# Kernel optimization log

Hardware: AMD Instinct MI355X
Metric: run time of the kernel (lower is better)

Reference implementation:

```python
import jax, jax.numpy as jnp
import numpy as np

HEADS = 8
IH, IW = 32, 32
C_IN, C_OUT = 512, 512


def setup_inputs() -> dict:
    key = jax.random.key(0)
    k1, k2, k3, k4, k5 = jax.random.split(key, 5)
    B = 32
    n = IH + IW + (IH // 2) * (IW // 2)  # pooled kv length = 320
    x = jax.random.normal(k1, (B, C_IN, IH, IW), dtype=jnp.float32)
    # 1x1 conv weights stored as [out, in] (bias-free qkv, biased output proj)
    Wqkv = jax.random.normal(k2, (3 * C_IN, C_IN), dtype=jnp.float32) * 0.02
    Wout = jax.random.normal(k3, (C_OUT, C_IN), dtype=jnp.float32) * 0.02
    bout = jnp.zeros((C_OUT,), dtype=jnp.float32)
    pos_embed = jax.random.normal(k4, (1, IH * IW, n), dtype=jnp.float32) * 0.2
    return {"x": x, "Wqkv": Wqkv, "Wout": Wout, "bout": bout, "pos_embed": pos_embed}


def _pool_gate(t, B, C, H, W):
    # adaptive_avg_pool2d(.,(None,1)) == mean over width -> [B,C,H]
    th = t.mean(axis=3)
    # adaptive_avg_pool2d(.,(1,None)) (+permute) == mean over height -> [B,C,W]
    tw = t.mean(axis=2)
    # adaptive_avg_pool2d to (H//2, W//2) with even dims == 2x2 average pooling
    tp = t.reshape(B, C, H // 2, 2, W // 2, 2).mean(axis=(3, 5)).reshape(B, C, -1)
    s = jax.nn.sigmoid(jnp.concatenate([th, tw, tp], axis=2))  # [B,C,n]
    d = C // HEADS
    # 'b (h d) n -> b h n d'
    return s.reshape(B, HEADS, d, -1).transpose(0, 1, 3, 2)


def reference(x, Wqkv, Wout, bout, pos_embed):
    B, C, H, W = x.shape
    d = C // HEADS
    scale = d ** (-0.5)
    qkv = jnp.einsum('bchw,oc->bohw', x, Wqkv)  # 1x1 conv, no bias
    q, k, v = jnp.split(qkv, 3, axis=1)
    # 'b (h d) ih iw -> b h (ih iw) d'
    q = q.reshape(B, HEADS, d, H * W).transpose(0, 1, 3, 2)
    k = _pool_gate(k, B, C, H, W)  # [B,h,n,d]
    v = _pool_gate(v, B, C, H, W)  # [B,h,n,d]
    dots = jnp.einsum('bhsd,bhnd->bhsn', q, k) * scale + pos_embed  # pos_embed [1,s,n] broadcasts
    attn = jax.nn.softmax(dots, axis=-1)
    out = jnp.einsum('bhsn,bhnd->bhsd', attn, v)
    # 'b h (ih iw) d -> b (h d) ih iw'
    out = out.transpose(0, 1, 3, 2).reshape(B, HEADS * d, H, W)
    out = jnp.einsum('bchw,oc->bohw', out, Wout) + bout[None, :, None, None]
    return out
```

## Files before the change

kernel.cpp:

```cpp
#include <hip/hip_runtime.h>
#include <hip/hip_bf16.h>
#include <math.h>

#define HEADS 8
#define CH    512
#define S     1024
#define NKV   320
#define DH    64
#define BATCH 32

typedef __attribute__((ext_vector_type(8))) short short8;
typedef __attribute__((ext_vector_type(4))) short short4v;
typedef __attribute__((ext_vector_type(4))) float float4v;
typedef __attribute__((ext_vector_type(4))) unsigned int uint4v;

__device__ __forceinline__ short f2bf(float f) {
    __hip_bfloat16 h = __float2bfloat16(f);
    return *reinterpret_cast<short*>(&h);
}

#define GLOAD_LDS16(gp, lp) __builtin_amdgcn_global_load_lds( \
    (const __attribute__((address_space(1))) void*)(gp),      \
    (__attribute__((address_space(3))) void*)(lp), 16, 0, 0)

__global__ __launch_bounds__(256) void pool_kernel(const float* __restrict__ x,
                                                   float* __restrict__ xp) {
    __shared__ float sm[4][1024];
    const int w = threadIdx.x >> 6;
    const int l = threadIdx.x & 63;
    const int p = blockIdx.x * 4 + w;
    const float* src = x + (size_t)p * 1024;
    #pragma unroll
    for (int j = 0; j < 16; ++j) sm[w][j * 64 + l] = src[j * 64 + l];
    __syncthreads();
    float* dst = xp + (size_t)p * NKV;
    const float* pl = sm[w];
    #pragma unroll
    for (int g = 0; g < 5; ++g) {
        const int nn = g * 64 + l;
        float r;
        if (nn < 32) {
            const int h = nn; float s = 0.f;
            #pragma unroll
            for (int ww = 0; ww < 32; ++ww) s += pl[h * 32 + ww];
            r = s * (1.0f / 32.0f);
        } else if (nn < 64) {
            const int ww = nn - 32; float s = 0.f;
            #pragma unroll
            for (int h = 0; h < 32; ++h) s += pl[h * 32 + ww];
            r = s * (1.0f / 32.0f);
        } else {
            const int i = nn - 64;
            const int ph = i >> 4, pw = i & 15;
            r = 0.25f * (pl[(2 * ph) * 32 + 2 * pw]     + pl[(2 * ph) * 32 + 2 * pw + 1] +
                         pl[(2 * ph + 1) * 32 + 2 * pw] + pl[(2 * ph + 1) * 32 + 2 * pw + 1]);
        }
        dst[nn] = r;
    }
}

__global__ __launch_bounds__(256) void tcast(const float* __restrict__ in,
                                             short* __restrict__ out, int R, int C) {
    __shared__ float sm[64][65];
    const int t = threadIdx.x;
    const int c0 = blockIdx.x * 64, r0 = blockIdx.y * 64;
    const float* ib = in + ((size_t)blockIdx.z * R + r0) * C + c0;
    #pragma unroll
    for (int rep = 0; rep < 4; ++rep) {
        const int r = rep * 16 + (t >> 4), c = (t & 15) * 4;
        const float4 v = *(const float4*)&ib[(size_t)r * C + c];
        sm[r][c] = v.x; sm[r][c + 1] = v.y; sm[r][c + 2] = v.z; sm[r][c + 3] = v.w;
    }
    __syncthreads();
    short* ob = out + ((size_t)blockIdx.z * C + c0) * R + r0;
    #pragma unroll
    for (int rep = 0; rep < 4; ++rep) {
        const int cr = rep * 16 + (t >> 4), rc = (t & 15) * 4;
        short4v p;
        #pragma unroll
        for (int e = 0; e < 4; ++e) p[e] = f2bf(sm[rc + e][cr]);
        *(short4v*)&ob[(size_t)cr * R + rc] = p;
    }
}

__global__ __launch_bounds__(256) void castw(const float* __restrict__ in,
                                             short* __restrict__ out, int n) {
    const int i = (blockIdx.x * 256 + threadIdx.x) * 4;
    if (i < n) {
        const float4 v = *(const float4*)&in[i];
        short4v p = {f2bf(v.x), f2bf(v.y), f2bf(v.z), f2bf(v.w)};
        *(short4v*)&out[i] = p;
    }
}

template <int MT, int NT, int ACT, typename OT>
__global__ __launch_bounds__(256) void gemm_bf16(const short* __restrict__ A, long sAb,
                                                 const short* __restrict__ B, long sBb,
                                                 const float* __restrict__ bias,
                                                 OT* __restrict__ C, int M, int N) {
    constexpr int K  = 512;
    constexpr int BM = 32 * MT, BN = 32 * NT;
    __shared__ short As[BM * 64];
    __shared__ short Bs[BN * 64];
    const int t = threadIdx.x, w = t >> 6, l = t & 63;
    const int wm = w >> 1, wn = w & 1, quad = l >> 4, m15 = l & 15;
    const int bz = blockIdx.z;
    const int n0 = blockIdx.x * BN, m0 = blockIdx.y * BM;
    const short* gA = A + (size_t)sAb * bz + (size_t)m0 * K;
    const short* gB = B + (size_t)sBb * bz + (size_t)n0 * K;
    const int lrow = l >> 3;
    const int pc   = l & 7;

    const float4v zf = {0.f, 0.f, 0.f, 0.f};
    float4v acc[MT][NT];
    #pragma unroll
    for (int i = 0; i < MT; ++i)
        #pragma unroll
        for (int j = 0; j < NT; ++j) acc[i][j] = zf;

    for (int k0 = 0; k0 < K; k0 += 64) {
        #pragma unroll
        for (int ii = w; ii < BM / 8; ii += 4) {
            const int row = ii * 8 + lrow;
            const int x = pc ^ (row & 7);
            GLOAD_LDS16(gA + (size_t)row * K + k0 + x * 8, &As[ii * 512]);
        }
        #pragma unroll
        for (int ii = w; ii < BN / 8; ii += 4) {
            const int row = ii * 8 + lrow;
            const int x = pc ^ (row & 7);
            GLOAD_LDS16(gB + (size_t)row * K + k0 + x * 8, &Bs[ii * 512]);
        }
        __syncthreads();
        #pragma unroll
        for (int ks = 0; ks < 2; ++ks) {
            const int xa = (((ks * 4 + quad) ^ (m15 & 7))) * 8;
            short8 aF[MT], bF[NT];
            #pragma unroll
            for (int i = 0; i < MT; ++i)
                aF[i] = *(const short8*)&As[((wm * MT + i) * 16 + m15) * 64 + xa];
            #pragma unroll
            for (int j = 0; j < NT; ++j)
                bF[j] = *(const short8*)&Bs[((wn * NT + j) * 16 + m15) * 64 + xa];
            #pragma unroll
            for (int i = 0; i < MT; ++i)
                #pragma unroll
                for (int j = 0; j < NT; ++j)
                    acc[i][j] = __builtin_amdgcn_mfma_f32_16x16x32_bf16(aF[i], bF[j], acc[i][j], 0, 0, 0);
        }
        __syncthreads();
    }

    OT* gC = C + (size_t)bz * M * N;
    #pragma unroll
    for (int i = 0; i < MT; ++i) {
        #pragma unroll
        for (int r = 0; r < 4; ++r) {
            const int row = m0 + (wm * MT + i) * 16 + quad * 4 + r;
            float bv = 0.f;
            if (ACT == 2) bv = bias[row];
            #pragma unroll
            for (int j = 0; j < NT; ++j) {
                const int col = n0 + (wn * NT + j) * 16 + m15;
                float v = acc[i][j][r];
                if (ACT == 1) { v = 1.0f / (1.0f + __expf(-v)); if (col < 512) v *= 0.125f; }
                if (ACT == 2) v += bv;
                if constexpr (sizeof(OT) == 2)
                    ((short*)gC)[(size_t)row * N + col] = f2bf(v);
                else
                    ((float*)gC)[(size_t)row * N + col] = v;
            }
        }
    }
}

__global__ __launch_bounds__(512, 6) void attn_mfma(const short* __restrict__ qT,
                                                    const short* __restrict__ kvT,
                                                    const float* __restrict__ pos,
                                                    short* __restrict__ aoT) {
    __shared__ short smB[64 * 320];
    const int tid = threadIdx.x, w = tid >> 6, l = tid & 63;
    const int quad = l >> 4, m15 = l & 15;
    const int b = blockIdx.z, h = blockIdx.y, s0 = blockIdx.x * 128;
    const short* kvb = kvT + (size_t)b * NKV * 1024;

    const int nperm = (l & 35) | ((l & 12) << 1) | ((l & 16) >> 2);
    #pragma unroll
    for (int i2 = w; i2 < 40; i2 += 8) {
        const int nb = i2 % 5, dg = i2 / 5;
        GLOAD_LDS16(kvb + (size_t)(nb * 64 + nperm) * 1024 + h * 64 + dg * 8,
                    &smB[(dg * 320 + nb * 64) * 8]);
    }
    const short* qb = qT + (size_t)(b * S + s0 + w * 16 + m15) * 512 + h * 64;
    const short8 aQ0 = *(const short8*)&qb[quad * 8];
    const short8 aQ1 = *(const short8*)&qb[32 + quad * 8];
    __syncthreads();

    const float* posrow = pos + (size_t)(s0 + w * 16 + m15) * NKV + quad * 8;
    unsigned int P[40];
    float lpart = 0.f;
    #pragma unroll
    for (int tt = 0; tt < 20; ++tt) {
        float4v a = {0.f, 0.f, 0.f, 0.f};
        const short8 k0 = *(const short8*)&smB[(quad * 320 + tt * 16 + m15) * 8];
        const short8 k1 = *(const short8*)&smB[((4 + quad) * 320 + tt * 16 + m15) * 8];
        a = __builtin_amdgcn_mfma_f32_16x16x32_bf16(k0, aQ0, a, 0, 0, 0);
        a = __builtin_amdgcn_mfma_f32_16x16x32_bf16(k1, aQ1, a, 0, 0, 0);
        const int n0 = (tt >> 2) * 64 + ((tt >> 1) & 1) * 32 + (tt & 1) * 4;
        const float4 pv = *(const float4*)&posrow[n0];
        const float p0 = __expf(a[0] + pv.x);
        const float p1 = __expf(a[1] + pv.y);
        const float p2 = __expf(a[2] + pv.z);
        const float p3 = __expf(a[3] + pv.w);
        lpart += (p0 + p1) + (p2 + p3);
        P[tt * 2]     = (unsigned int)(unsigned short)f2bf(p0) |
                        ((unsigned int)(unsigned short)f2bf(p1) << 16);
        P[tt * 2 + 1] = (unsigned int)(unsigned short)f2bf(p2) |
                        ((unsigned int)(unsigned short)f2bf(p3) << 16);
    }

    float lrow = lpart;
    lrow += __shfl_xor(lrow, 16, 64);
    lrow += __shfl_xor(lrow, 32, 64);
    const float invl = 1.0f / lrow;
    float inv[4];
    #pragma unroll
    for (int r = 0; r < 4; ++r)
        inv[r] = __shfl(invl, (l & 48) | (quad * 4 + r), 64);

    __syncthreads();

    for (int it = 0; it < 5; ++it) {
        const int i2 = it * 512 + tid;
        const int n5 = i2 & 31, d8 = (i2 >> 5) & 7, nb = i2 >> 8;
        const int n = nb * 32 + n5;
        const short8 v = *(const short8*)&kvb[(size_t)n * 1024 + 512 + h * 64 + d8 * 8];
        const int x = n >> 3;
        #pragma unroll
        for (int e = 0; e < 8; ++e)
            smB[(d8 * 8 + e) * 320 + ((x ^ e) * 8) + (n & 7)] = v[e];
    }
    __syncthreads();

    const float4v zf = {0.f, 0.f, 0.f, 0.f};
    #pragma unroll
    for (int half = 0; half < 2; ++half) {
        float4v O0 = zf, O1 = zf;
        #pragma unroll
        for (int c = 0; c < 5; ++c) {
            const uint4v u0 = {P[c * 8 + 0], P[c * 8 + 1], P[c * 8 + 2], P[c * 8 + 3]};
            const uint4v u1 = {P[c * 8 + 4], P[c * 8 + 5], P[c * 8 + 6], P[c * 8 + 7]};
            const short8 aP0 = __builtin_bit_cast(short8, u0);
            const short8 aP1 = __builtin_bit_cast(short8, u1);
            #pragma unroll
            for (int ks = 0; ks < 2; ++ks) {
                const int xr = (c * 8 + ks * 4 + quad) ^ (m15 & 7);
                const int dt0 = half * 2;
                const short8 bV0 = *(const short8*)&smB[(dt0 * 16 + m15) * 320 + xr * 8];
                const short8 bV1 = *(const short8*)&smB[((dt0 + 1) * 16 + m15) * 320 + xr * 8];
                if (ks == 0) {
                    O0 = __builtin_amdgcn_mfma_f32_16x16x32_bf16(aP0, bV0, O0, 0, 0, 0);
                    O1 = __builtin_amdgcn_mfma_f32_16x16x32_bf16(aP0, bV1, O1, 0, 0, 0);
                } else {
                    O0 = __builtin_amdgcn_mfma_f32_16x16x32_bf16(aP1, bV0, O0, 0, 0, 0);
                    O1 = __builtin_amdgcn_mfma_f32_16x16x32_bf16(aP1, bV1, O1, 0, 0, 0);
                }
            }
        }
        #pragma unroll
        for (int r = 0; r < 4; ++r) {
            const int s = s0 + w * 16 + quad * 4 + r;
            short* orow = &aoT[(size_t)(b * S + s) * 512 + h * 64 + (half * 2) * 16 + m15];
            orow[0]  = f2bf(O0[r] * inv[r]);
            orow[16] = f2bf(O1[r] * inv[r]);
        }
    }
}

extern "C" void kernel_launch(void* const* d_in, const int* in_sizes, int n_in,
                              void* d_out, int out_size, void* d_ws, size_t ws_size,
                              hipStream_t stream) {
    const float* x    = (const float*)d_in[0];
    const float* Wqkv = (const float*)d_in[1];
    const float* Wout = (const float*)d_in[2];
    const float* bout = (const float*)d_in[3];
    const float* pos  = (const float*)d_in[4];
    char* ws = (char*)d_ws;
    float* xp   = (float*)(ws + 0);
    short* xT   = (short*)(ws + 20971520);
    short* xpT  = (short*)(ws + 54525952);
    short* qT   = (short*)(ws + 65011712);
    short* kvT  = (short*)(ws + 98566144);
    short* aoT  = (short*)(ws + 119537664);
    short* Wbf  = (short*)(ws + 153092096);
    short* Wobf = (short*)(ws + 154664960);
    float* out  = (float*)d_out;

    castw<<<dim3(768), 256, 0, stream>>>(Wqkv, Wbf, 1536 * 512);
    castw<<<dim3(256), 256, 0, stream>>>(Wout, Wobf, 512 * 512);
    pool_kernel<<<dim3(BATCH * CH / 4), 256, 0, stream>>>(x, xp);
    tcast<<<dim3(16, 8, BATCH), 256, 0, stream>>>(x, xT, CH, S);
    tcast<<<dim3(5, 8, BATCH), 256, 0, stream>>>(xp, xpT, CH, NKV);
    gemm_bf16<4, 4, 0, short><<<dim3(4, 8, BATCH), 256, 0, stream>>>(
        xT, (long)S * CH, Wbf, 0, nullptr, qT, S, CH);
    gemm_bf16<2, 8, 1, short><<<dim3(4, 5, BATCH), 256, 0, stream>>>(
        xpT, (long)NKV * CH, Wbf + CH * CH, 0, nullptr, kvT, NKV, 2 * CH);
    attn_mfma<<<dim3(8, HEADS, BATCH), 512, 0, stream>>>(qT, kvT, pos, aoT);
    gemm_bf16<4, 4, 2, float><<<dim3(8, 4, BATCH), 256, 0, stream>>>(
        Wobf, 0, aoT, (long)S * CH, bout, out, CH, S);
}
```

Before: 298.1 us.

## Reuse K/V LDS tiles across four query tiles per attention block and use exp2

Each attention block now handles 512 query rows in a loop of four 128-row sub-tiles. K and V are staged into separate shared arrays once per block instead of once per 128 rows, and the next Q fragment is prefetched during the current iteration. The log2(e) factor is folded into the Q projection epilogue, so softmax uses a native exp2 with one fma for the positional term. The kernel uses more shared memory per block and a lower launch-bounds occupancy hint, and the grid has a quarter as many blocks, which reduces parallelism.

```diff
diff --git a/kernel.cpp b/kernel.cpp
--- a/kernel.cpp
+++ b/kernel.cpp
@@ -17,6 +17,14 @@
 __device__ __forceinline__ short f2bf(float f) {
     __hip_bfloat16 h = __float2bfloat16(f);
     return *reinterpret_cast<short*>(&h);
+}
+
+__device__ __forceinline__ float fexp2(float x) {
+#if __has_builtin(__builtin_amdgcn_exp2f)
+    return __builtin_amdgcn_exp2f(x);
+#else
+    return exp2f(x);
+#endif
 }
 
 #define GLOAD_LDS16(gp, lp) __builtin_amdgcn_global_load_lds( \
@@ -165,6 +173,7 @@
                 float v = acc[i][j][r];
                 if (ACT == 1) { v = 1.0f / (1.0f + __expf(-v)); if (col < 512) v *= 0.125f; }
                 if (ACT == 2) v += bv;
+                if (ACT == 3) v *= 1.4426950408889634f;
                 if constexpr (sizeof(OT) == 2)
                     ((short*)gC)[(size_t)row * N + col] = f2bf(v);
                 else
@@ -174,106 +183,126 @@
     }
 }
 
-__global__ __launch_bounds__(512, 6) void attn_mfma(const short* __restrict__ qT,
+__global__ __launch_bounds__(512, 4) void attn_mfma(const short* __restrict__ qT,
                                                     const short* __restrict__ kvT,
                                                     const float* __restrict__ pos,
                                                     short* __restrict__ aoT) {
-    __shared__ short smB[64 * 320];
+    __shared__ short smK[8 * 320 * 8];
+    __shared__ short smV[64 * 320];
     const int tid = threadIdx.x, w = tid >> 6, l = tid & 63;
     const int quad = l >> 4, m15 = l & 15;
-    const int b = blockIdx.z, h = blockIdx.y, s0 = blockIdx.x * 128;
+    const int b = blockIdx.z, h = blockIdx.y, s0 = blockIdx.x * 512;
     const short* kvb = kvT + (size_t)b * NKV * 1024;
-
-    const int nperm = (l & 35) | ((l & 12) << 1) | ((l & 16) >> 2);
-    #pragma unroll
-    for (int i2 = w; i2 < 40; i2 += 8) {
-        const int nb = i2 % 5, dg = i2 / 5;
-        GLOAD_LDS16(kvb + (size_t)(nb * 64 + nperm) * 1024 + h * 64 + dg * 8,
-                    &smB[(dg * 320 + nb * 64) * 8]);
-    }
-    const short* qb = qT + (size_t)(b * S + s0 + w * 16 + m15) * 512 + h * 64;
-    const short8 aQ0 = *(const short8*)&qb[quad * 8];
-    const short8 aQ1 = *(const short8*)&qb[32 + quad * 8];
-    __syncthreads();
-
-    const float* posrow = pos + (size_t)(s0 + w * 16 + m15) * NKV + quad * 8;
-    unsigned int P[40];
-    float lpart = 0.f;
-    #pragma unroll
-    for (int tt = 0; tt < 20; ++tt) {
-        float4v a = {0.f, 0.f, 0.f, 0.f};
-        const short8 k0 = *(const short8*)&smB[(quad * 320 + tt * 16 + m15) * 8];
-        const short8 k1 = *(const short8*)&smB[((4 + quad) * 320 + tt * 16 + m15) * 8];
-        a = __builtin_amdgcn_mfma_f32_16x16x32_bf16(k0, aQ0, a, 0, 0, 0);
-        a = __builtin_amdgcn_mfma_f32_16x16x32_bf16(k1, aQ1, a, 0, 0, 0);
-        const int n0 = (tt >> 2) * 64 + ((tt >> 1) & 1) * 32 + (tt & 1) * 4;
-        const float4 pv = *(const float4*)&posrow[n0];
-        const float p0 = __expf(a[0] + pv.x);
-        const float p1 = __expf(a[1] + pv.y);
-        const float p2 = __expf(a[2] + pv.z);
-        const float p3 = __expf(a[3] + pv.w);
-        lpart += (p0 + p1) + (p2 + p3);
-        P[tt * 2]     = (unsigned int)(unsigned short)f2bf(p0) |
-                        ((unsigned int)(unsigned short)f2bf(p1) << 16);
-        P[tt * 2 + 1] = (unsigned int)(unsigned short)f2bf(p2) |
-                        ((unsigned int)(unsigned short)f2bf(p3) << 16);
-    }
-
-    float lrow = lpart;
-    lrow += __shfl_xor(lrow, 16, 64);
-    lrow += __shfl_xor(lrow, 32, 64);
-    const float invl = 1.0f / lrow;
-    float inv[4];
-    #pragma unroll
-    for (int r = 0; r < 4; ++r)
-        inv[r] = __shfl(invl, (l & 48) | (quad * 4 + r), 64);
-
-    __syncthreads();
-
+    constexpr float LOG2E = 1.4426950408889634f;
+
+    short8 vreg[5];
+    #pragma unroll
     for (int it = 0; it < 5; ++it) {
         const int i2 = it * 512 + tid;
         const int n5 = i2 & 31, d8 = (i2 >> 5) & 7, nb = i2 >> 8;
         const int n = nb * 32 + n5;
-        const short8 v = *(const short8*)&kvb[(size_t)n * 1024 + 512 + h * 64 + d8 * 8];
+        vreg[it] = *(const short8*)&kvb[(size_t)n * 1024 + 512 + h * 64 + d8 * 8];
+    }
+    const int nperm = (l & 35) | ((l & 12) << 1) | ((l & 16) >> 2);
+    #pragma unroll
+    for (int i2 = w; i2 < 40; i2 += 8) {
+        const int nb = i2 % 5, dg = i2 / 5;
+        GLOAD_LDS16(kvb + (size_t)(nb * 64 + nperm) * 1024 + h * 64 + dg * 8,
+                    &smK[(dg * 320 + nb * 64) * 8]);
+    }
+    #pragma unroll
+    for (int it = 0; it < 5; ++it) {
+        const int i2 = it * 512 + tid;
+        const int n5 = i2 & 31, d8 = (i2 >> 5) & 7, nb = i2 >> 8;
+        const int n = nb * 32 + n5;
         const int x = n >> 3;
         #pragma unroll
         for (int e = 0; e < 8; ++e)
-            smB[(d8 * 8 + e) * 320 + ((x ^ e) * 8) + (n & 7)] = v[e];
-    }
+            smV[(d8 * 8 + e) * 320 + ((x ^ e) * 8) + (n & 7)] = vreg[it][e];
+    }
+
+    const short* qbase = qT + (size_t)(b * S + s0 + w * 16 + m15) * 512 + h * 64;
+    short8 cq0 = *(const short8*)&qbase[quad * 8];
+    short8 cq1 = *(const short8*)&qbase[32 + quad * 8];
+
     __syncthreads();
 
     const float4v zf = {0.f, 0.f, 0.f, 0.f};
-    #pragma unroll
-    for (int half = 0; half < 2; ++half) {
-        float4v O0 = zf, O1 = zf;
-        #pragma unroll
-        for (int c = 0; c < 5; ++c) {
-            const uint4v u0 = {P[c * 8 + 0], P[c * 8 + 1], P[c * 8 + 2], P[c * 8 + 3]};
-            const uint4v u1 = {P[c * 8 + 4], P[c * 8 + 5], P[c * 8 + 6], P[c * 8 + 7]};
-            const short8 aP0 = __builtin_bit_cast(short8, u0);
-            const short8 aP1 = __builtin_bit_cast(short8, u1);
-            #pragma unroll
-            for (int ks = 0; ks < 2; ++ks) {
-                const int xr = (c * 8 + ks * 4 + quad) ^ (m15 & 7);
-                const int dt0 = half * 2;
-                const short8 bV0 = *(const short8*)&smB[(dt0 * 16 + m15) * 320 + xr * 8];
-                const short8 bV1 = *(const short8*)&smB[((dt0 + 1) * 16 + m15) * 320 + xr * 8];
-                if (ks == 0) {
-                    O0 = __builtin_amdgcn_mfma_f32_16x16x32_bf16(aP0, bV0, O0, 0, 0, 0);
-                    O1 = __builtin_amdgcn_mfma_f32_16x16x32_bf16(aP0, bV1, O1, 0, 0, 0);
-                } else {
-                    O0 = __builtin_amdgcn_mfma_f32_16x16x32_bf16(aP1, bV0, O0, 0, 0, 0);
-                    O1 = __builtin_amdgcn_mfma_f32_16x16x32_bf16(aP1, bV1, O1, 0, 0, 0);
+    #pragma unroll 1
+    for (int si = 0; si < 4; ++si) {
+        short8 nq0, nq1;
+        if (si < 3) {
+            const short* nqb = qbase + (size_t)(si + 1) * 128 * 512;
+            nq0 = *(const short8*)&nqb[quad * 8];
+            nq1 = *(const short8*)&nqb[32 + quad * 8];
+        }
+
+        const float* posrow = pos + (size_t)(s0 + si * 128 + w * 16 + m15) * NKV + quad * 8;
+        unsigned int P[40];
+        float lpart = 0.f;
+        #pragma unroll
+        for (int tt = 0; tt < 20; ++tt) {
+            float4v a = zf;
+            const short8 k0 = *(const short8*)&smK[(quad * 320 + tt * 16 + m15) * 8];
+            const short8 k1 = *(const short8*)&smK[((4 + quad) * 320 + tt * 16 + m15) * 8];
+            a = __builtin_amdgcn_mfma_f32_16x16x32_bf16(k0, cq0, a, 0, 0, 0);
+            a = __builtin_amdgcn_mfma_f32_16x16x32_bf16(k1, cq1, a, 0, 0, 0);
+            const int n0 = (tt >> 2) * 64 + ((tt >> 1) & 1) * 32 + (tt & 1) * 4;
+            const float4 pv = *(const float4*)&posrow[n0];
+            const float p0 = fexp2(fmaf(pv.x, LOG2E, a[0]));
+            const float p1 = fexp2(fmaf(pv.y, LOG2E, a[1]));
+            const float p2 = fexp2(fmaf(pv.z, LOG2E, a[2]));
+            const float p3 = fexp2(fmaf(pv.w, LOG2E, a[3]));
+            lpart += (p0 + p1) + (p2 + p3);
+            P[tt * 2]     = (unsigned int)(unsigned short)f2bf(p0) |
+                            ((unsigned int)(unsigned short)f2bf(p1) << 16);
+            P[tt * 2 + 1] = (unsigned int)(unsigned short)f2bf(p2) |
+                            ((unsigned int)(unsigned short)f2bf(p3) << 16);
+        }
+
+        float lrow = lpart;
+        lrow += __shfl_xor(lrow, 16, 64);
+        lrow += __shfl_xor(lrow, 32, 64);
+        const float invl = 1.0f / lrow;
+        float inv[4];
+        #pragma unroll
+        for (int r = 0; r < 4; ++r)
+            inv[r] = __shfl(invl, (l & 48) | (quad * 4 + r), 64);
+
+        #pragma unroll
+        for (int half = 0; half < 2; ++half) {
+            float4v O0 = zf, O1 = zf;
+            #pragma unroll
+            for (int c = 0; c < 5; ++c) {
+                const uint4v u0 = {P[c * 8 + 0], P[c * 8 + 1], P[c * 8 + 2], P[c * 8 + 3]};
+                const uint4v u1 = {P[c * 8 + 4], P[c * 8 + 5], P[c * 8 + 6], P[c * 8 + 7]};
+                const short8 aP0 = __builtin_bit_cast(short8, u0);
+                const short8 aP1 = __builtin_bit_cast(short8, u1);
+                #pragma unroll
+                for (int ks = 0; ks < 2; ++ks) {
+                    const int xr = (c * 8 + ks * 4 + quad) ^ (m15 & 7);
+                    const int dt0 = half * 2;
+                    const short8 bV0 = *(const short8*)&smV[(dt0 * 16 + m15) * 320 + xr * 8];
+                    const short8 bV1 = *(const short8*)&smV[((dt0 + 1) * 16 + m15) * 320 + xr * 8];
+                    if (ks == 0) {
+                        O0 = __builtin_amdgcn_mfma_f32_16x16x32_bf16(aP0, bV0, O0, 0, 0, 0);
+                        O1 = __builtin_amdgcn_mfma_f32_16x16x32_bf16(aP0, bV1, O1, 0, 0, 0);
+                    } else {
+                        O0 = __builtin_amdgcn_mfma_f32_16x16x32_bf16(aP1, bV0, O0, 0, 0, 0);
+                        O1 = __builtin_amdgcn_mfma_f32_16x16x32_bf16(aP1, bV1, O1, 0, 0, 0);
+                    }
                 }
             }
-        }
-        #pragma unroll
-        for (int r = 0; r < 4; ++r) {
-            const int s = s0 + w * 16 + quad * 4 + r;
-            short* orow = &aoT[(size_t)(b * S + s) * 512 + h * 64 + (half * 2) * 16 + m15];
-            orow[0]  = f2bf(O0[r] * inv[r]);
-            orow[16] = f2bf(O1[r] * inv[r]);
-        }
+            #pragma unroll
+            for (int r = 0; r < 4; ++r) {
+                const int s = s0 + si * 128 + w * 16 + quad * 4 + r;
+                short* orow = &aoT[(size_t)(b * S + s) * 512 + h * 64 + (half * 2) * 16 + m15];
+                orow[0]  = f2bf(O0[r] * inv[r]);
+                orow[16] = f2bf(O1[r] * inv[r]);
+            }
+        }
+
+        if (si < 3) { cq0 = nq0; cq1 = nq1; }
     }
 }
 
@@ -301,11 +330,11 @@
     pool_kernel<<<dim3(BATCH * CH / 4), 256, 0, stream>>>(x, xp);
     tcast<<<dim3(16, 8, BATCH), 256, 0, stream>>>(x, xT, CH, S);
     tcast<<<dim3(5, 8, BATCH), 256, 0, stream>>>(xp, xpT, CH, NKV);
-    gemm_bf16<4, 4, 0, short><<<dim3(4, 8, BATCH), 256, 0, stream>>>(
+    gemm_bf16<4, 4, 3, short><<<dim3(4, 8, BATCH), 256, 0, stream>>>(
         xT, (long)S * CH, Wbf, 0, nullptr, qT, S, CH);
     gemm_bf16<2, 8, 1, short><<<dim3(4, 5, BATCH), 256, 0, stream>>>(
         xpT, (long)NKV * CH, Wbf + CH * CH, 0, nullptr, kvT, NKV, 2 * CH);
-    attn_mfma<<<dim3(8, HEADS, BATCH), 512, 0, stream>>>(qT, kvT, pos, aoT);
+    attn_mfma<<<dim3(2, HEADS, BATCH), 512, 0, stream>>>(qT, kvT, pos, aoT);
     gemm_bf16<4, 4, 2, float><<<dim3(8, 4, BATCH), 256, 0, stream>>>(
         Wobf, 0, aoT, (long)S * CH, bout, out, CH, S);
 }
```

Result: slower. 582.5 us (+95.4%).
